# Kernel tuning notes

Hardware: AMD Instinct MI355X
Metric: run time of the kernel (lower is better)

Reference implementation:

```python
import jax, jax.numpy as jnp
import numpy as np

D_MODEL = 1024
MEM_SIZE = 131072
TOP_K = 64
D_STATE = 16
D_CONV = 4
D_INNER = 2 * D_MODEL          # expand=2
DT_RANK = (D_MODEL + 15) // 16  # ceil(d_model/16) = 64
EPS_COS = 1e-8
EPS_LN = 1e-5


def setup_inputs() -> dict:
    key = jax.random.key(0)
    ks = jax.random.split(key, 12)
    s = 0.02
    inp = {
        "query": jax.random.normal(ks[0], (D_MODEL,), jnp.float32),
        "memory": jax.random.normal(ks[1], (MEM_SIZE, D_MODEL), jnp.float32),
        "memory_usage": jnp.zeros((MEM_SIZE,), jnp.int32),
        # Mamba block params
        "in_proj_w": jax.random.normal(ks[2], (2 * D_INNER, D_MODEL), jnp.float32) * s,
        "conv_w": jax.random.normal(ks[3], (D_INNER, D_CONV), jnp.float32) * s,
        "conv_b": jnp.zeros((D_INNER,), jnp.float32),
        "x_proj_w": jax.random.normal(ks[4], (DT_RANK + 2 * D_STATE, D_INNER), jnp.float32) * s,
        "dt_proj_w": jax.random.normal(ks[5], (D_INNER, DT_RANK), jnp.float32) * s,
        "dt_proj_b": jax.random.normal(ks[6], (D_INNER,), jnp.float32) * s,
        "A_log": jnp.log(jnp.broadcast_to(jnp.arange(1, D_STATE + 1, dtype=jnp.float32), (D_INNER, D_STATE))),
        "D": jnp.ones((D_INNER,), jnp.float32),
        "out_proj_w": jax.random.normal(ks[7], (D_MODEL, D_INNER), jnp.float32) * s,
        # LayerNorm params
        "ln_g": jnp.ones((D_MODEL,), jnp.float32),
        "ln_b": jnp.zeros((D_MODEL,), jnp.float32),
    }
    return inp


def _mamba(x, in_proj_w, conv_w, conv_b, x_proj_w, dt_proj_w, dt_proj_b, A_log, D, out_proj_w):
    # x: (B, L, d_model)
    B, L, _ = x.shape
    xz = jnp.einsum("bld,ed->ble", x, in_proj_w)            # (B, L, 2*d_inner)
    u, z = jnp.split(xz, 2, axis=-1)                          # each (B, L, d_inner)
    # depthwise causal conv1d, kernel D_CONV
    up = jnp.pad(u, ((0, 0), (D_CONV - 1, 0), (0, 0)))
    uc = sum(up[:, j:j + L, :] * conv_w[:, j] for j in range(D_CONV)) + conv_b
    u = jax.nn.silu(uc)
    x_dbl = jnp.einsum("bld,ed->ble", u, x_proj_w)           # (B, L, dt_rank+2*d_state)
    dt = x_dbl[..., :DT_RANK]
    Bm = x_dbl[..., DT_RANK:DT_RANK + D_STATE]               # (B, L, d_state)
    Cm = x_dbl[..., DT_RANK + D_STATE:]                      # (B, L, d_state)
    delta = jax.nn.softplus(jnp.einsum("blr,dr->bld", dt, dt_proj_w) + dt_proj_b)  # (B, L, d_inner)
    A = -jnp.exp(A_log)                                       # (d_inner, d_state)
    deltaA = jnp.exp(delta[..., None] * A)                    # (B, L, d_inner, d_state)
    dBu = delta[..., None] * Bm[:, :, None, :] * u[..., None]

    def step(h, inputs):
        dA_t, dBu_t, C_t = inputs                             # (B,d,s),(B,d,s),(B,s)
        h = dA_t * h + dBu_t
        y = jnp.einsum("bds,bs->bd", h, C_t)
        return h, y

    h0 = jnp.zeros((B, D_INNER, D_STATE), x.dtype)
    xs = (jnp.swapaxes(deltaA, 0, 1), jnp.swapaxes(dBu, 0, 1), jnp.swapaxes(Cm, 0, 1))
    _, ys = jax.lax.scan(step, h0, xs)                        # (L, B, d_inner)
    y = jnp.swapaxes(ys, 0, 1) + u * D
    y = y * jax.nn.silu(z)
    return jnp.einsum("bld,ed->ble", y, out_proj_w)          # (B, L, d_model)


def reference(query, memory, memory_usage, in_proj_w, conv_w, conv_b, x_proj_w,
              dt_proj_w, dt_proj_b, A_log, D, out_proj_w, ln_g, ln_b):
    # cosine similarity of query vs every memory row (torch eps semantics)
    dots = memory @ query                                     # (MEM,)
    denom = jnp.maximum(jnp.linalg.norm(memory, axis=1) * jnp.linalg.norm(query), EPS_COS)
    sims = dots / denom
    _, idx = jax.lax.top_k(sims, TOP_K)
    retrieved = memory[idx]                                   # (k, d_model)
    usage_new = memory_usage.at[idx].add(1)
    seq = retrieved[None]                                     # (1, k, d_model)
    processed = _mamba(seq, in_proj_w, conv_w, conv_b, x_proj_w,
                       dt_proj_w, dt_proj_b, A_log, D, out_proj_w)
    ctx = processed[:, -1, :]                                 # (1, d_model)
    mu = jnp.mean(ctx, axis=-1, keepdims=True)
    var = jnp.var(ctx, axis=-1, keepdims=True)
    out = (ctx - mu) * jax.lax.rsqrt(var + EPS_LN) * ln_g + ln_b
    return out, usage_new
```

## Files before the change

### kernel.cpp

```cpp
#include <hip/hip_runtime.h>
#include <math.h>

#define D_MODEL   1024
#define MEM_SIZE  131072
#define TOP_K     64
#define D_STATE   16
#define D_CONV    4
#define D_INNER   2048
#define DT_RANK   64

#define WS_CAND1   0u
#define WS_CAND2   131072u
#define WS_IDXF    139264u
#define WS_U       139520u
#define WS_US      663808u
#define WS_XDBL    1188096u
#define WS_DELTA   1212672u
#define WS_Z63     1736960u
#define WS_YFIN    1745152u
#define WS_CTX     1753344u

__device__ __forceinline__ float wave_reduce_add(float v) {
#pragma unroll
  for (int off = 32; off > 0; off >>= 1) v += __shfl_xor(v, off, 64);
  return v;
}

__device__ __forceinline__ unsigned long long pack_key(float sim, int idx) {
  unsigned int fb = __float_as_uint(sim);
  fb = (fb & 0x80000000u) ? ~fb : (fb | 0x80000000u);
  return ((unsigned long long)fb << 32) | (unsigned int)(~(unsigned int)idx);
}

template <int N>
__device__ __forceinline__ void bitonic_sort_desc(unsigned long long* keys, int tid) {
  for (int k = 2; k <= N; k <<= 1) {
    for (int j = k >> 1; j > 0; j >>= 1) {
      for (int i = tid; i < N; i += 256) {
        int ixj = i ^ j;
        if (ixj > i) {
          unsigned long long a = keys[i], b = keys[ixj];
          bool desc = ((i & k) == 0);
          if (desc ? (a < b) : (a > b)) { keys[i] = b; keys[ixj] = a; }
        }
      }
      __syncthreads();
    }
  }
}

__global__ __launch_bounds__(256) void k_sims(const float* __restrict__ mem,
                                              const float* __restrict__ query,
                                              unsigned long long* __restrict__ cand1) {
  __shared__ float red[4];
  __shared__ unsigned long long keys[512];
  const int tid = threadIdx.x, lane = tid & 63, wave = tid >> 6;

  const float4* q4 = (const float4*)query;
  float4 qf[4];
  float qs = 0.f;
#pragma unroll
  for (int c = 0; c < 4; ++c) {
    qf[c] = q4[c * 64 + lane];
    qs += qf[c].x * qf[c].x + qf[c].y * qf[c].y + qf[c].z * qf[c].z + qf[c].w * qf[c].w;
  }
  qs = wave_reduce_add(qs);
  if (lane == 0) red[wave] = qs;
  __syncthreads();
  const float qn = sqrtf(red[0] + red[1] + red[2] + red[3]);

  const float4* m4 = (const float4*)mem;
  const int base = blockIdx.x * 512 + wave * 128;
  for (int it = 0; it < 64; ++it) {
    const int r0 = base + it * 2, r1 = r0 + 1;
    float d0 = 0.f, s0 = 0.f, d1 = 0.f, s1 = 0.f;
#pragma unroll
    for (int c = 0; c < 4; ++c) {
      float4 a = m4[r0 * 256 + c * 64 + lane];
      float4 b = m4[r1 * 256 + c * 64 + lane];
      d0 += a.x * qf[c].x + a.y * qf[c].y + a.z * qf[c].z + a.w * qf[c].w;
      s0 += a.x * a.x + a.y * a.y + a.z * a.z + a.w * a.w;
      d1 += b.x * qf[c].x + b.y * qf[c].y + b.z * qf[c].z + b.w * qf[c].w;
      s1 += b.x * b.x + b.y * b.y + b.z * b.z + b.w * b.w;
    }
    d0 = wave_reduce_add(d0); s0 = wave_reduce_add(s0);
    d1 = wave_reduce_add(d1); s1 = wave_reduce_add(s1);
    if (lane == 0) {
      float sim0 = d0 / fmaxf(sqrtf(s0) * qn, 1e-8f);
      float sim1 = d1 / fmaxf(sqrtf(s1) * qn, 1e-8f);
      keys[wave * 128 + it * 2]     = pack_key(sim0, r0);
      keys[wave * 128 + it * 2 + 1] = pack_key(sim1, r1);
    }
  }
  __syncthreads();
  bitonic_sort_desc<512>(keys, tid);
  if (tid < 64) cand1[blockIdx.x * 64 + tid] = keys[tid];
}

__global__ __launch_bounds__(256) void k_merge16(const unsigned long long* __restrict__ in,
                                                 unsigned long long* __restrict__ outk) {
  __shared__ unsigned long long keys[1024];
  const int tid = threadIdx.x;
  for (int i = tid; i < 1024; i += 256) keys[i] = in[blockIdx.x * 1024 + i];
  __syncthreads();
  bitonic_sort_desc<1024>(keys, tid);
  if (tid < 64) outk[blockIdx.x * 64 + tid] = keys[tid];
}

__global__ __launch_bounds__(256) void k_usage(const int* __restrict__ usage_in,
                                               float* __restrict__ usage_out) {
  const int i = blockIdx.x * 256 + threadIdx.x;
  usage_out[i] = (float)usage_in[i];
}

__global__ __launch_bounds__(256) void k_final(const unsigned long long* __restrict__ in,
                                               int* __restrict__ idxf,
                                               float* __restrict__ usage_out) {
  __shared__ unsigned long long keys[1024];
  const int tid = threadIdx.x;
  for (int i = tid; i < 1024; i += 256) keys[i] = in[i];
  __syncthreads();
  bitonic_sort_desc<1024>(keys, tid);
  if (tid < 64) {
    unsigned int low = (unsigned int)(keys[tid] & 0xFFFFFFFFull);
    int idx = (int)(~low);
    idxf[tid] = idx;
    usage_out[idx] += 1.0f;
  }
}

__global__ __launch_bounds__(256) void k_inproj(const float* __restrict__ mem,
                                                const float* __restrict__ inw,
                                                const int* __restrict__ idxf,
                                                float* __restrict__ u,
                                                float* __restrict__ z63) {
  const int tid = threadIdx.x, lane = tid & 63, wave = tid >> 6;
  const int bid = blockIdx.x;
  const float4* m4 = (const float4*)mem;
  const float4* w4 = (const float4*)inw;
  if (bid < 256) {
    const int e0 = bid * 8 + wave * 2;
    float4 wa[4], wb[4];
#pragma unroll
    for (int c = 0; c < 4; ++c) {
      wa[c] = w4[e0 * 256 + c * 64 + lane];
      wb[c] = w4[(e0 + 1) * 256 + c * 64 + lane];
    }
    for (int l = 0; l < 64; ++l) {
      const int r = idxf[l];
      float da = 0.f, db = 0.f;
#pragma unroll
      for (int c = 0; c < 4; ++c) {
        float4 x = m4[r * 256 + c * 64 + lane];
        da += x.x * wa[c].x + x.y * wa[c].y + x.z * wa[c].z + x.w * wa[c].w;
        db += x.x * wb[c].x + x.y * wb[c].y + x.z * wb[c].z + x.w * wb[c].w;
      }
      da = wave_reduce_add(da);
      db = wave_reduce_add(db);
      if (lane == 0) {
        u[l * 2048 + e0]     = da;
        u[l * 2048 + e0 + 1] = db;
      }
    }
  } else {
    const int wid = (bid - 256) * 4 + wave;
    const int r63 = idxf[63];
    float4 xf[4];
#pragma unroll
    for (int c = 0; c < 4; ++c) xf[c] = m4[r63 * 256 + c * 64 + lane];
    for (int j = 0; j < 16; ++j) {
      const int e = 2048 + wid * 16 + j;
      float dsum = 0.f;
#pragma unroll
      for (int c = 0; c < 4; ++c) {
        float4 w = w4[e * 256 + c * 64 + lane];
        dsum += w.x * xf[c].x + w.y * xf[c].y + w.z * xf[c].z + w.w * xf[c].w;
      }
      dsum = wave_reduce_add(dsum);
      if (lane == 0) z63[e - 2048] = dsum;
    }
  }
}

__global__ __launch_bounds__(256) void k_conv(const float* __restrict__ u,
                                              const float* __restrict__ cw,
                                              const float* __restrict__ cb,
                                              float* __restrict__ us) {
  const int e = blockIdx.x * 256 + threadIdx.x;
  const int l = blockIdx.y;
  float acc = cb[e];
#pragma unroll
  for (int j = 0; j < 4; ++j) {
    const int li = l - 3 + j;
    if (li >= 0) acc += u[li * 2048 + e] * cw[e * 4 + j];
  }
  us[l * 2048 + e] = acc / (1.f + __expf(-acc));
}

__global__ __launch_bounds__(256) void k_xproj(const float* __restrict__ us,
                                               const float* __restrict__ xw,
                                               float* __restrict__ xdbl) {
  __shared__ __align__(16) float su[2048];
  const int tid = threadIdx.x, lane = tid & 63, wave = tid >> 6;
  const int l = blockIdx.x;
  for (int i = tid; i < 2048; i += 256) su[i] = us[l * 2048 + i];
  __syncthreads();
  const float4* su4 = (const float4*)su;
  const float4* xw4 = (const float4*)xw;
  for (int j = wave; j < 96; j += 4) {
    float dsum = 0.f;
#pragma unroll
    for (int c = 0; c < 8; ++c) {
      float4 a = su4[c * 64 + lane];
      float4 w = xw4[j * 512 + c * 64 + lane];
      dsum += a.x * w.x + a.y * w.y + a.z * w.z + a.w * w.w;
    }
    dsum = wave_reduce_add(dsum);
    if (lane == 0) xdbl[l * 96 + j] = dsum;
  }
}

__global__ __launch_bounds__(256) void k_dtproj(const float* __restrict__ xdbl,
                                                const float* __restrict__ dtw,
                                                const float* __restrict__ dtb,
                                                float* __restrict__ delta) {
  const int d = blockIdx.x * 256 + threadIdx.x;
  const int l0 = blockIdx.y * 8;
  float w[64];
  const float4* dtw4 = (const float4*)dtw;
#pragma unroll
  for (int c = 0; c < 16; ++c) {
    float4 t = dtw4[d * 16 + c];
    w[c * 4] = t.x; w[c * 4 + 1] = t.y; w[c * 4 + 2] = t.z; w[c * 4 + 3] = t.w;
  }
  const float b = dtb[d];
  for (int l = 0; l < 8; ++l) {
    float acc = b;
    const float* arow = xdbl + (l0 + l) * 96;
#pragma unroll
    for (int r = 0; r < 64; ++r) acc += w[r] * arow[r];
    float sp = fmaxf(acc, 0.f) + log1pf(__expf(-fabsf(acc)));
    delta[(l0 + l) * 2048 + d] = sp;
  }
}

__global__ __launch_bounds__(256) void k_scan(const float* __restrict__ delta,
                                              const float* __restrict__ us,
                                              const float* __restrict__ xdbl,
                                              const float* __restrict__ A_log,
                                              const float* __restrict__ Dp,
                                              const float* __restrict__ z63,
                                              float* __restrict__ yfin) {
  const int t = blockIdx.x * 256 + threadIdx.x;
  const int d = t >> 4, s = t & 15;
  const float A = -__expf(A_log[t]);
  float h = 0.f;
#pragma unroll 8
  for (int l = 0; l < 64; ++l) {
    float dl = delta[l * 2048 + d];
    float ul = us[l * 2048 + d];
    float bl = xdbl[l * 96 + 64 + s];
    h = __expf(dl * A) * h + dl * bl * ul;
  }
  float v = h * xdbl[63 * 96 + 80 + s];
#pragma unroll
  for (int off = 8; off >= 1; off >>= 1) v += __shfl_xor(v, off, 64);
  if (s == 0) {
    float y = v + us[63 * 2048 + d] * Dp[d];
    float z = z63[d];
    yfin[d] = y * (z / (1.f + __expf(-z)));
  }
}

__global__ __launch_bounds__(256) void k_outproj(const float* __restrict__ yfin,
                                                 const float* __restrict__ ow,
                                                 float* __restrict__ ctx) {
  const int tid = threadIdx.x, lane = tid & 63, wave = tid >> 6;
  const int m = blockIdx.x * 4 + wave;
  const float4* y4 = (const float4*)yfin;
  const float4* ow4 = (const float4*)ow;
  float dsum = 0.f;
#pragma unroll
  for (int c = 0; c < 8; ++c) {
    float4 w = ow4[m * 512 + c * 64 + lane];
    float4 y = y4[c * 64 + lane];
    dsum += w.x * y.x + w.y * y.y + w.z * y.z + w.w * y.w;
  }
  dsum = wave_reduce_add(dsum);
  if (lane == 0) ctx[m] = dsum;
}

__global__ __launch_bounds__(256) void k_ln(const float* __restrict__ ctx,
                                            const float* __restrict__ g,
                                            const float* __restrict__ b,
                                            float* __restrict__ out) {
  __shared__ float red[8];
  const int tid = threadIdx.x, lane = tid & 63, wave = tid >> 6;
  float4 v = ((const float4*)ctx)[tid];
  float s1 = v.x + v.y + v.z + v.w;
  float s2 = v.x * v.x + v.y * v.y + v.z * v.z + v.w * v.w;
  s1 = wave_reduce_add(s1);
  s2 = wave_reduce_add(s2);
  if (lane == 0) { red[wave] = s1; red[4 + wave] = s2; }
  __syncthreads();
  const float mu = (red[0] + red[1] + red[2] + red[3]) * (1.f / 1024.f);
  const float var = (red[4] + red[5] + red[6] + red[7]) * (1.f / 1024.f) - mu * mu;
  const float rs = rsqrtf(var + 1e-5f);
  const int i0 = tid * 4;
  out[i0 + 0] = (v.x - mu) * rs * g[i0 + 0] + b[i0 + 0];
  out[i0 + 1] = (v.y - mu) * rs * g[i0 + 1] + b[i0 + 1];
  out[i0 + 2] = (v.z - mu) * rs * g[i0 + 2] + b[i0 + 2];
  out[i0 + 3] = (v.w - mu) * rs * g[i0 + 3] + b[i0 + 3];
}

extern "C" void kernel_launch(void* const* d_in, const int* in_sizes, int n_in,
                              void* d_out, int out_size, void* d_ws, size_t ws_size,
                              hipStream_t stream) {
  const float* query    = (const float*)d_in[0];
  const float* memory   = (const float*)d_in[1];
  const int*   usage_in = (const int*)d_in[2];
  const float* in_proj  = (const float*)d_in[3];
  const float* conv_w   = (const float*)d_in[4];
  const float* conv_b   = (const float*)d_in[5];
  const float* x_proj   = (const float*)d_in[6];
  const float* dt_proj  = (const float*)d_in[7];
  const float* dt_bias  = (const float*)d_in[8];
  const float* A_log    = (const float*)d_in[9];
  const float* Dp       = (const float*)d_in[10];
  const float* out_proj = (const float*)d_in[11];
  const float* ln_g     = (const float*)d_in[12];
  const float* ln_b     = (const float*)d_in[13];

  char* ws = (char*)d_ws;
  unsigned long long* cand1 = (unsigned long long*)(ws + WS_CAND1);
  unsigned long long* cand2 = (unsigned long long*)(ws + WS_CAND2);
  int*   idxf  = (int*)(ws + WS_IDXF);
  float* u     = (float*)(ws + WS_U);
  float* us_   = (float*)(ws + WS_US);
  float* xdbl  = (float*)(ws + WS_XDBL);
  float* delta = (float*)(ws + WS_DELTA);
  float* z63   = (float*)(ws + WS_Z63);
  float* yfin  = (float*)(ws + WS_YFIN);
  float* ctx   = (float*)(ws + WS_CTX);

  float* out_ln    = (float*)d_out;
  float* usage_out = (float*)d_out + 1024;

  hipLaunchKernelGGL(k_sims,    dim3(256), dim3(256), 0, stream, memory, query, cand1);
  hipLaunchKernelGGL(k_merge16, dim3(16),  dim3(256), 0, stream, cand1, cand2);
  hipLaunchKernelGGL(k_usage,   dim3(512), dim3(256), 0, stream, usage_in, usage_out);
  hipLaunchKernelGGL(k_final,   dim3(1),   dim3(256), 0, stream, cand2, idxf, usage_out);
  hipLaunchKernelGGL(k_inproj,  dim3(288), dim3(256), 0, stream, memory, in_proj, idxf, u, z63);
  hipLaunchKernelGGL(k_conv,    dim3(8, 64), dim3(256), 0, stream, u, conv_w, conv_b, us_);
  hipLaunchKernelGGL(k_xproj,   dim3(64),  dim3(256), 0, stream, us_, x_proj, xdbl);
  hipLaunchKernelGGL(k_dtproj,  dim3(8, 8), dim3(256), 0, stream, xdbl, dt_proj, dt_bias, delta);
  hipLaunchKernelGGL(k_scan,    dim3(128), dim3(256), 0, stream, delta, us_, xdbl, A_log, Dp, z63, yfin);
  hipLaunchKernelGGL(k_outproj, dim3(256), dim3(256), 0, stream, yfin, out_proj, ctx);
  hipLaunchKernelGGL(k_ln,      dim3(1),   dim3(256), 0, stream, ctx, ln_g, ln_b, out_ln);
}
```

Before: 935.1 us.

## Double similarity grid, fuse usage copy, use nontemporal loads, add merge stage

The cosine-similarity kernel now launches 512 blocks of 256 rows each instead of 256 blocks of 512 rows, so more blocks are in flight to saturate bandwidth on the 512 MB memory scan. Each wave processes four rows per iteration using nontemporal vector loads, which raises memory-level parallelism and avoids polluting cache. The usage int-to-float copy is folded into the similarity kernel, removing one launch. The top-k reduction gains an extra merge stage (32 then 2 blocks, then a final 128-key sort), adding one small launch in exchange.

```diff
diff --git a/kernel.cpp b/kernel.cpp
--- a/kernel.cpp
+++ b/kernel.cpp
@@ -10,20 +10,27 @@
 #define DT_RANK   64
 
 #define WS_CAND1   0u
-#define WS_CAND2   131072u
-#define WS_IDXF    139264u
-#define WS_U       139520u
-#define WS_US      663808u
-#define WS_XDBL    1188096u
-#define WS_DELTA   1212672u
-#define WS_Z63     1736960u
-#define WS_YFIN    1745152u
-#define WS_CTX     1753344u
+#define WS_CAND2   262144u
+#define WS_CAND3   278528u
+#define WS_IDXF    279552u
+#define WS_U       294912u
+#define WS_US      819200u
+#define WS_XDBL    1343488u
+#define WS_DELTA   1368064u
+#define WS_Z63     1892352u
+#define WS_YFIN    1900544u
+#define WS_CTX     1908736u
+
+typedef float vfloat4 __attribute__((ext_vector_type(4)));
 
 __device__ __forceinline__ float wave_reduce_add(float v) {
 #pragma unroll
   for (int off = 32; off > 0; off >>= 1) v += __shfl_xor(v, off, 64);
   return v;
+}
+
+__device__ __forceinline__ vfloat4 ld_nt(const float* p) {
+  return __builtin_nontemporal_load((const vfloat4*)p);
 }
 
 __device__ __forceinline__ unsigned long long pack_key(float sim, int idx) {
@@ -51,10 +58,17 @@
 
 __global__ __launch_bounds__(256) void k_sims(const float* __restrict__ mem,
                                               const float* __restrict__ query,
+                                              const int* __restrict__ usage_in,
+                                              float* __restrict__ usage_out,
                                               unsigned long long* __restrict__ cand1) {
   __shared__ float red[4];
-  __shared__ unsigned long long keys[512];
-  const int tid = threadIdx.x, lane = tid & 63, wave = tid >> 6;
+  __shared__ unsigned long long keys[256];
+  const int tid = threadIdx.x, lane = tid & 63, wave = tid >> 6;
+
+  {
+    const int gi = blockIdx.x * 256 + tid;
+    usage_out[gi] = (float)usage_in[gi];
+  }
 
   const float4* q4 = (const float4*)query;
   float4 qf[4];
@@ -69,31 +83,34 @@
   __syncthreads();
   const float qn = sqrtf(red[0] + red[1] + red[2] + red[3]);
 
-  const float4* m4 = (const float4*)mem;
-  const int base = blockIdx.x * 512 + wave * 128;
-  for (int it = 0; it < 64; ++it) {
-    const int r0 = base + it * 2, r1 = r0 + 1;
-    float d0 = 0.f, s0 = 0.f, d1 = 0.f, s1 = 0.f;
+  const int base = blockIdx.x * 256 + wave * 64;
+  for (int it = 0; it < 16; ++it) {
+    const int r0 = base + it * 4;
+    float d[4] = {0.f, 0.f, 0.f, 0.f}, s[4] = {0.f, 0.f, 0.f, 0.f};
 #pragma unroll
     for (int c = 0; c < 4; ++c) {
-      float4 a = m4[r0 * 256 + c * 64 + lane];
-      float4 b = m4[r1 * 256 + c * 64 + lane];
-      d0 += a.x * qf[c].x + a.y * qf[c].y + a.z * qf[c].z + a.w * qf[c].w;
-      s0 += a.x * a.x + a.y * a.y + a.z * a.z + a.w * a.w;
-      d1 += b.x * qf[c].x + b.y * qf[c].y + b.z * qf[c].z + b.w * qf[c].w;
-      s1 += b.x * b.x + b.y * b.y + b.z * b.z + b.w * b.w;
-    }
-    d0 = wave_reduce_add(d0); s0 = wave_reduce_add(s0);
-    d1 = wave_reduce_add(d1); s1 = wave_reduce_add(s1);
+#pragma unroll
+      for (int k = 0; k < 4; ++k) {
+        vfloat4 a = ld_nt(mem + (size_t)(r0 + k) * 1024 + c * 256 + lane * 4);
+        d[k] += a.x * qf[c].x + a.y * qf[c].y + a.z * qf[c].z + a.w * qf[c].w;
+        s[k] += a.x * a.x + a.y * a.y + a.z * a.z + a.w * a.w;
+      }
+    }
+#pragma unroll
+    for (int k = 0; k < 4; ++k) {
+      d[k] = wave_reduce_add(d[k]);
+      s[k] = wave_reduce_add(s[k]);
+    }
     if (lane == 0) {
-      float sim0 = d0 / fmaxf(sqrtf(s0) * qn, 1e-8f);
-      float sim1 = d1 / fmaxf(sqrtf(s1) * qn, 1e-8f);
-      keys[wave * 128 + it * 2]     = pack_key(sim0, r0);
-      keys[wave * 128 + it * 2 + 1] = pack_key(sim1, r1);
-    }
-  }
-  __syncthreads();
-  bitonic_sort_desc<512>(keys, tid);
+#pragma unroll
+      for (int k = 0; k < 4; ++k) {
+        float sim = d[k] / fmaxf(sqrtf(s[k]) * qn, 1e-8f);
+        keys[wave * 64 + it * 4 + k] = pack_key(sim, r0 + k);
+      }
+    }
+  }
+  __syncthreads();
+  bitonic_sort_desc<256>(keys, tid);
   if (tid < 64) cand1[blockIdx.x * 64 + tid] = keys[tid];
 }
 
@@ -107,20 +124,14 @@
   if (tid < 64) outk[blockIdx.x * 64 + tid] = keys[tid];
 }
 
-__global__ __launch_bounds__(256) void k_usage(const int* __restrict__ usage_in,
-                                               float* __restrict__ usage_out) {
-  const int i = blockIdx.x * 256 + threadIdx.x;
-  usage_out[i] = (float)usage_in[i];
-}
-
 __global__ __launch_bounds__(256) void k_final(const unsigned long long* __restrict__ in,
                                                int* __restrict__ idxf,
                                                float* __restrict__ usage_out) {
-  __shared__ unsigned long long keys[1024];
+  __shared__ unsigned long long keys[128];
   const int tid = threadIdx.x;
-  for (int i = tid; i < 1024; i += 256) keys[i] = in[i];
-  __syncthreads();
-  bitonic_sort_desc<1024>(keys, tid);
+  if (tid < 128) keys[tid] = in[tid];
+  __syncthreads();
+  bitonic_sort_desc<128>(keys, tid);
   if (tid < 64) {
     unsigned int low = (unsigned int)(keys[tid] & 0xFFFFFFFFull);
     int idx = (int)(~low);
@@ -334,6 +345,7 @@
   char* ws = (char*)d_ws;
   unsigned long long* cand1 = (unsigned long long*)(ws + WS_CAND1);
   unsigned long long* cand2 = (unsigned long long*)(ws + WS_CAND2);
+  unsigned long long* cand3 = (unsigned long long*)(ws + WS_CAND3);
   int*   idxf  = (int*)(ws + WS_IDXF);
   float* u     = (float*)(ws + WS_U);
   float* us_   = (float*)(ws + WS_US);
@@ -346,10 +358,10 @@
   float* out_ln    = (float*)d_out;
   float* usage_out = (float*)d_out + 1024;
 
-  hipLaunchKernelGGL(k_sims,    dim3(256), dim3(256), 0, stream, memory, query, cand1);
-  hipLaunchKernelGGL(k_merge16, dim3(16),  dim3(256), 0, stream, cand1, cand2);
-  hipLaunchKernelGGL(k_usage,   dim3(512), dim3(256), 0, stream, usage_in, usage_out);
-  hipLaunchKernelGGL(k_final,   dim3(1),   dim3(256), 0, stream, cand2, idxf, usage_out);
+  hipLaunchKernelGGL(k_sims,    dim3(512), dim3(256), 0, stream, memory, query, usage_in, usage_out, cand1);
+  hipLaunchKernelGGL(k_merge16, dim3(32),  dim3(256), 0, stream, cand1, cand2);
+  hipLaunchKernelGGL(k_merge16, dim3(2),   dim3(256), 0, stream, cand2, cand3);
+  hipLaunchKernelGGL(k_final,   dim3(1),   dim3(256), 0, stream, cand3, idxf, usage_out);
   hipLaunchKernelGGL(k_inproj,  dim3(288), dim3(256), 0, stream, memory, in_proj, idxf, u, z63);
   hipLaunchKernelGGL(k_conv,    dim3(8, 64), dim3(256), 0, stream, u, conv_w, conv_b, us_);
   hipLaunchKernelGGL(k_xproj,   dim3(64),  dim3(256), 0, stream, us_, x_proj, xdbl);
```

New measurement: 900.2 us. 1.04x faster.
